# Performance work log

Measured on AMD Instinct MI355X. Metric: run time of the kernel, lower is better.

The kernel has to match this reference:

```python
import jax, jax.numpy as jnp
import numpy as np

HEADS = 7
DIM_HEAD = 64
SCALE = DIM_HEAD ** -0.5


def setup_inputs() -> dict:
    key = jax.random.key(0)
    ks = jax.random.split(key, 6)
    b, n, dim = 8, 1024, 448
    inner = HEADS * DIM_HEAD  # 448
    x = jax.random.normal(ks[0], (b, n, dim), dtype=jnp.float32)
    w_qv = jax.random.normal(ks[1], (dim, 2 * inner), dtype=jnp.float32) * 0.02
    ext_k = jax.random.normal(ks[2], (HEADS, n, DIM_HEAD), dtype=jnp.float32)
    ext_bias = jax.random.normal(ks[3], (HEADS, n, n), dtype=jnp.float32)
    w_out = jax.random.normal(ks[4], (inner, dim), dtype=jnp.float32) * 0.02
    b_out = jnp.zeros((dim,), dtype=jnp.float32)
    return {"x": x, "w_qv": w_qv, "ext_k": ext_k, "ext_bias": ext_bias,
            "w_out": w_out, "b_out": b_out}


def reference(x, w_qv, ext_k, ext_bias, w_out, b_out):
    b, n, dim = x.shape
    qv = x @ w_qv                                   # [b, n, 2*inner]
    q, v = jnp.split(qv, 2, axis=-1)
    # b n (h d) -> b h n d
    q = q.reshape(b, n, HEADS, DIM_HEAD).transpose(0, 2, 1, 3)
    v = v.reshape(b, n, HEADS, DIM_HEAD).transpose(0, 2, 1, 3)
    # scores vs external learned key, additive bias applied BEFORE scale
    dots = (jnp.einsum('bhnd,hmd->bhnm', q, ext_k) + ext_bias[None]) * SCALE
    attn = jax.nn.softmax(dots, axis=-1)
    out = jnp.einsum('bhnm,bhmd->bhnd', attn, v)
    out = out.transpose(0, 2, 1, 3).reshape(b, n, HEADS * DIM_HEAD)
    return out @ w_out + b_out  # dropout is identity in eval mode
```

## Files before the change

### kernel.cpp

```cpp
#include <hip/hip_runtime.h>
#include <hip/hip_bf16.h>
#include <hip/hip_fp16.h>

#define BATCH 8
#define NSEQ 1024
#define DIMM 448
#define NHEAD 7
#define HDIM 64
#define MROWS (BATCH*NSEQ)
#define KDIM 448
#define SCALE_F 0.125f

typedef short short8 __attribute__((ext_vector_type(8)));
typedef float floatx16 __attribute__((ext_vector_type(16)));

#define MFMA32(a,b,c) __builtin_amdgcn_mfma_f32_32x32x16_bf16(a,b,c,0,0,0)

__device__ __forceinline__ unsigned short f2bf(float f){
    __hip_bfloat16 h = __float2bfloat16(f);
    return *reinterpret_cast<unsigned short*>(&h);
}
__device__ __forceinline__ float bf2f(unsigned short u){
    __hip_bfloat16 h; *reinterpret_cast<unsigned short*>(&h) = u;
    return __bfloat162float(h);
}
__device__ __forceinline__ float h2f(unsigned short u){
    __half h; *reinterpret_cast<unsigned short*>(&h) = u;
    return __half2float(h);
}
__device__ __forceinline__ unsigned short f2h(float f){
    __half h = __float2half(f);
    return *reinterpret_cast<unsigned short*>(&h);
}

__global__ __launch_bounds__(256)
void prep_all(const float* __restrict__ x, const float* __restrict__ ek,
              const float* __restrict__ wqv, const float* __restrict__ wout,
              const float* __restrict__ eb,
              unsigned short* __restrict__ xh, unsigned short* __restrict__ ekh,
              unsigned short* __restrict__ wqvTh, unsigned short* __restrict__ woTh,
              unsigned short* __restrict__ woTl, unsigned short* __restrict__ bp)
{
    __shared__ float T[2][64][33];
    const int bx = blockIdx.x, tid = threadIdx.x;

    if (bx < 3584) {
        int i = bx*256 + tid;
        float4 v = ((const float4*)x)[i];
        ((ushort4*)xh)[i] = make_ushort4(f2bf(v.x), f2bf(v.y), f2bf(v.z), f2bf(v.w));
    } else if (bx < 4032) {
        int i = (bx-3584)*256 + tid;
        float4 v = ((const float4*)ek)[i];
        ((ushort4*)ekh)[i] = make_ushort4(f2bf(v.x), f2bf(v.y), f2bf(v.z), f2bf(v.w));
    } else if (bx < 4228) {
        int lid = (bx-4032)*4 + (tid>>6);
        int kc = lid % 56, ng = lid / 56;
        int n = ng*64 + (tid&63);
        unsigned short h[8];
#pragma unroll
        for (int j = 0; j < 8; ++j) h[j] = f2bf(wqv[(size_t)(kc*8+j)*896 + n]);
        size_t o = (size_t)n*KDIM + kc*8;
        *(ushort4*)(wqvTh + o)     = make_ushort4(h[0],h[1],h[2],h[3]);
        *(ushort4*)(wqvTh + o + 4) = make_ushort4(h[4],h[5],h[6],h[7]);
    } else if (bx < 4340) {
        int lid = (bx-4228)*4 + (tid>>6);
        int kc = lid % 56, ng = lid / 56;
        int n = ng*64 + (tid&63);
        ushort4 h0={0,0,0,0}, h1={0,0,0,0}, l0={0,0,0,0}, l1={0,0,0,0};
        if (n < DIMM) {
            unsigned short h[8], l[8];
#pragma unroll
            for (int j = 0; j < 8; ++j) {
                float f = wout[(size_t)(kc*8+j)*DIMM + n];
                h[j] = f2bf(f); l[j] = f2bf(f - bf2f(h[j]));
            }
            h0 = make_ushort4(h[0],h[1],h[2],h[3]); h1 = make_ushort4(h[4],h[5],h[6],h[7]);
            l0 = make_ushort4(l[0],l[1],l[2],l[3]); l1 = make_ushort4(l[4],l[5],l[6],l[7]);
        }
        size_t o = (size_t)n*KDIM + kc*8;
        *(ushort4*)(woTh + o) = h0; *(ushort4*)(woTh + o + 4) = h1;
        *(ushort4*)(woTl + o) = l0; *(ushort4*)(woTl + o + 4) = l1;
    } else {
        const int sub = tid >> 7, st = tid & 127;
        const int lid = (bx-4340)*2 + sub;
        const int mt = lid & 31, qt = (lid>>5) & 15, h = lid >> 9;
#pragma unroll
        for (int it = 0; it < 4; ++it) {
            int idx = it*128 + st;
            int row = idx >> 3, c4 = (idx & 7)*4;
            float4 v = *(const float4*)(eb + ((size_t)(h*NSEQ + qt*64 + row))*NSEQ + mt*32 + c4);
            T[sub][row][c4+0]=v.x; T[sub][row][c4+1]=v.y;
            T[sub][row][c4+2]=v.z; T[sub][row][c4+3]=v.w;
        }
        __syncthreads();
        const int g2 = st >> 6, lane = st & 63;
        const int lq = lane & 31, quad = lane >> 5;
        const int q = g2*32 + lq;
        unsigned short* dst = bp + ((((size_t)h*16 + qt)*32 + mt)*4 + g2*2)*512 + lane*8;
#pragma unroll
        for (int jj = 0; jj < 2; ++jj) {
            unsigned short o[8];
#pragma unroll
            for (int t = 0; t < 8; ++t) {
                int m = (t&3) + 8*(t>>2) + 16*jj + 4*quad;
                o[t] = f2h(T[sub][q][m] * SCALE_F);
            }
            *(ushort4*)(dst + jj*512)     = make_ushort4(o[0],o[1],o[2],o[3]);
            *(ushort4*)(dst + jj*512 + 4) = make_ushort4(o[4],o[5],o[6],o[7]);
        }
    }
}

__global__ __launch_bounds__(64, 2)
void gemm1_reg(const unsigned short* __restrict__ Ah, const unsigned short* __restrict__ Bh,
               unsigned short* __restrict__ qd, unsigned short* __restrict__ vTd)
{
    const int lane = threadIdx.x;
    const int lq = lane & 31, lh = lane >> 5;
    const int m0 = blockIdx.x * 64;
    const int y  = blockIdx.y;
    const int n0 = y * 64;
    const unsigned short* aB = Ah + (size_t)(m0 + lq)*KDIM + lh*8;
    const unsigned short* bB = Bh + (size_t)(n0 + lq)*KDIM + lh*8;

    floatx16 acc[2][2] = {};
    short8 aR[2][2][2], bR[2][2][2];
#define LD1(kt, par) {                                                        \
    _Pragma("unroll") for (int fm = 0; fm < 2; ++fm)                          \
    _Pragma("unroll") for (int c = 0; c < 2; ++c) {                           \
        aR[par][fm][c] = *(const short8*)(aB + (size_t)fm*32*KDIM + (kt)*32 + c*16); \
        bR[par][fm][c] = *(const short8*)(bB + (size_t)fm*32*KDIM + (kt)*32 + c*16); } }

    LD1(0, 0)
#pragma unroll
    for (int kt = 0; kt < 14; ++kt) {
        const int par = kt & 1;
        if (kt < 13) LD1(kt+1, par^1)
#pragma unroll
        for (int c = 0; c < 2; ++c)
#pragma unroll
            for (int fm = 0; fm < 2; ++fm)
#pragma unroll
                for (int fn = 0; fn < 2; ++fn)
                    acc[fm][fn] = MFMA32(aR[par][fm][c], bR[par][fn][c], acc[fm][fn]);
    }
#undef LD1

    if (y < NHEAD) {
#pragma unroll
        for (int fm = 0; fm < 2; ++fm)
#pragma unroll
            for (int fn = 0; fn < 2; ++fn) {
                const int d = fn*32 + lq;
#pragma unroll
                for (int r = 0; r < 16; ++r) {
                    const int gm = m0 + fm*32 + (r&3) + 8*(r>>2) + 4*lh;
                    const int b = gm >> 10, ns = gm & 1023;
                    qd[((size_t)((b*NHEAD + y)*NSEQ + ns))*HDIM + d] = f2bf(acc[fm][fn][r]);
                }
            }
    } else {
        const int head = y - NHEAD;
#pragma unroll
        for (int fm = 0; fm < 2; ++fm)
#pragma unroll
            for (int fn = 0; fn < 2; ++fn) {
                const int d = fn*32 + lq;
#pragma unroll
                for (int r = 0; r < 16; ++r) {
                    const int gm = m0 + fm*32 + (r&3) + 8*(r>>2) + 4*lh;
                    const int b = gm >> 10, ns = gm & 1023;
                    vTd[((size_t)((b*NHEAD + head)*HDIM + d))*NSEQ + ns] = f2bf(acc[fm][fn][r]);
                }
            }
    }
}

__global__ __launch_bounds__(64, 2)
void attn4(const unsigned short* __restrict__ qh_g, const unsigned short* __restrict__ vTh,
           const unsigned short* __restrict__ ekh, const unsigned short* __restrict__ bp,
           unsigned short* __restrict__ aoh, unsigned short* __restrict__ aol)
{
    __shared__ unsigned short pS[1024];
    __shared__ float linv[2][32];

    const int lane = threadIdx.x;
    const int lq = lane & 31, lh = lane >> 5;
    const int qt = blockIdx.x, head = blockIdx.y, b = blockIdx.z;
    const int bh = b*NHEAD + head;

    short8 qf[2][4];
#pragma unroll
    for (int g2 = 0; g2 < 2; ++g2)
#pragma unroll
        for (int c = 0; c < 4; ++c)
            qf[g2][c] = *(const short8*)(qh_g +
                ((size_t)(bh*NSEQ) + qt*64 + g2*32 + lq)*HDIM + c*16 + lh*8);

    const unsigned short* kB = ekh + ((size_t)head*NSEQ + lq)*HDIM + lh*8;
    const unsigned short* vB = vTh + ((size_t)(bh*HDIM) + lq)*NSEQ;
    const unsigned short* bB = bp + ((size_t)(head*16 + qt))*65536 + lane*8;

    short8 kR[2][4], vR[2][4], bR[2][4];
#define PREF(J, par) { const int mm = ((J) < 32) ? (J) : 0;                    \
    _Pragma("unroll") for (int c = 0; c < 4; ++c)                              \
        kR[par][c] = *(const short8*)(kB + (size_t)mm*2048 + c*16);            \
    _Pragma("unroll") for (int c2 = 0; c2 < 2; ++c2)                           \
    _Pragma("unroll") for (int h2 = 0; h2 < 2; ++h2)                           \
        vR[par][c2*2+h2] = *(const short8*)(vB + (size_t)(h2*32)*NSEQ + mm*32 + (c2*2+lh)*8); \
    _Pragma("unroll") for (int u = 0; u < 4; ++u)                              \
        bR[par][u] = *(const short8*)(bB + ((size_t)mm*4 + u)*512); }

    floatx16 O[2][2] = {};
    float ls[2] = {0.f, 0.f};

#define SEC(J, par, nxt) {                                                     \
    PREF((J)+1, nxt)                                                           \
    _Pragma("unroll") for (int g2 = 0; g2 < 2; ++g2) {                         \
        floatx16 S = {};                                                       \
        _Pragma("unroll") for (int c = 0; c < 4; ++c)                          \
            S = MFMA32(kR[par][c], qf[g2][c], S);                              \
        _Pragma("unroll") for (int g = 0; g < 4; ++g) {                        \
            unsigned short hb[4];                                              \
            _Pragma("unroll") for (int j2 = 0; j2 < 4; ++j2) {                 \
                const int i = g*4 + j2;                                        \
                float bs = h2f((unsigned short)bR[par][g2*2 + (i>>3)][i&7]);   \
                float pv = __expf(fmaf(S[i], SCALE_F, bs));                    \
                ls[g2] += pv;  hb[j2] = f2bf(pv);                              \
            }                                                                  \
            *(ushort4*)(pS + g*256 + lq*8 + lh*4) = make_ushort4(hb[0],hb[1],hb[2],hb[3]); \
        }                                                                      \
        _Pragma("unroll") for (int c2 = 0; c2 < 2; ++c2) {                     \
            short8 pf = *(const short8*)(pS + ((c2*2+lh)*32 + lq)*8);          \
            O[g2][0] = MFMA32(pf, vR[par][c2*2+0], O[g2][0]);                  \
            O[g2][1] = MFMA32(pf, vR[par][c2*2+1], O[g2][1]);                  \
        } } }

    PREF(0, 0)
    for (int jj = 0; jj < 16; ++jj) {
        SEC(2*jj,   0, 1)
        SEC(2*jj+1, 1, 0)
    }
#undef SEC
#undef PREF

    float lt0 = ls[0] + __shfl_xor(ls[0], 32);
    float lt1 = ls[1] + __shfl_xor(ls[1], 32);
    if (lh == 0) { linv[0][lq] = 1.f/lt0; linv[1][lq] = 1.f/lt1; }

#pragma unroll
    for (int g2 = 0; g2 < 2; ++g2)
#pragma unroll
        for (int r = 0; r < 16; ++r) {
            const int qr = (r&3) + 8*(r>>2) + 4*lh;
            const float inv = linv[g2][qr];
            const size_t o = ((size_t)(b*NSEQ) + qt*64 + g2*32 + qr)*DIMM + head*HDIM + lq;
            float v0 = O[g2][0][r]*inv, v1 = O[g2][1][r]*inv;
            unsigned short h0 = f2bf(v0), h1 = f2bf(v1);
            aoh[o]      = h0;  aol[o]      = f2bf(v0 - bf2f(h0));
            aoh[o + 32] = h1;  aol[o + 32] = f2bf(v1 - bf2f(h1));
        }
}

__global__ __launch_bounds__(64, 2)
void gemm2_reg(const unsigned short* __restrict__ Ah, const unsigned short* __restrict__ Al,
               const unsigned short* __restrict__ Bh, const unsigned short* __restrict__ Bl,
               const float* __restrict__ bias, float* __restrict__ out)
{
    const int lane = threadIdx.x;
    const int lq = lane & 31, lh = lane >> 5;
    const int m0 = blockIdx.x * 64;
    const int n0 = blockIdx.y * 64;
    const unsigned short* aBh = Ah + (size_t)(m0 + lq)*KDIM + lh*8;
    const unsigned short* aBl = Al + (size_t)(m0 + lq)*KDIM + lh*8;
    const unsigned short* bBh = Bh + (size_t)(n0 + lq)*KDIM + lh*8;
    const unsigned short* bBl = Bl + (size_t)(n0 + lq)*KDIM + lh*8;

    floatx16 acc[2][2] = {};
    short8 aH[2][2][2], aL[2][2][2], bH[2][2][2], bL[2][2][2];
#define LD2(kt, par) {                                                        \
    _Pragma("unroll") for (int fm = 0; fm < 2; ++fm)                          \
    _Pragma("unroll") for (int c = 0; c < 2; ++c) {                           \
        const size_t off = (size_t)fm*32*KDIM + (kt)*32 + c*16;               \
        aH[par][fm][c] = *(const short8*)(aBh + off);                         \
        aL[par][fm][c] = *(const short8*)(aBl + off);                         \
        bH[par][fm][c] = *(const short8*)(bBh + off);                         \
        bL[par][fm][c] = *(const short8*)(bBl + off); } }

    LD2(0, 0)
#pragma unroll
    for (int kt = 0; kt < 14; ++kt) {
        const int par = kt & 1;
        if (kt < 13) LD2(kt+1, par^1)
#pragma unroll
        for (int c = 0; c < 2; ++c)
#pragma unroll
            for (int fm = 0; fm < 2; ++fm)
#pragma unroll
                for (int fn = 0; fn < 2; ++fn) {
                    acc[fm][fn] = MFMA32(aH[par][fm][c], bH[par][fn][c], acc[fm][fn]);
                    acc[fm][fn] = MFMA32(aL[par][fm][c], bH[par][fn][c], acc[fm][fn]);
                    acc[fm][fn] = MFMA32(aH[par][fm][c], bL[par][fn][c], acc[fm][fn]);
                }
    }
#undef LD2

#pragma unroll
    for (int fm = 0; fm < 2; ++fm)
#pragma unroll
        for (int fn = 0; fn < 2; ++fn) {
            const int gn = n0 + fn*32 + lq;
            const float bv = bias[gn];
#pragma unroll
            for (int r = 0; r < 16; ++r) {
                const int gm = m0 + fm*32 + (r&3) + 8*(r>>2) + 4*lh;
                out[(size_t)gm*DIMM + gn] = acc[fm][fn][r] + bv;
            }
        }
}

extern "C" void kernel_launch(void* const* d_in, const int* in_sizes, int n_in,
                              void* d_out, int out_size, void* d_ws, size_t ws_size,
                              hipStream_t stream)
{
    const float* x    = (const float*)d_in[0];
    const float* wqv  = (const float*)d_in[1];
    const float* ek   = (const float*)d_in[2];
    const float* eb   = (const float*)d_in[3];
    const float* wout = (const float*)d_in[4];
    const float* bout = (const float*)d_in[5];
    float* out = (float*)d_out;

    const size_t MK = (size_t)MROWS*KDIM;
    const size_t EK = (size_t)NHEAD*NSEQ*HDIM;
    unsigned short* p = (unsigned short*)d_ws;
    unsigned short* xh    = p;  p += MK;
    unsigned short* wqvTh = p;  p += (size_t)896*KDIM;
    unsigned short* woTh  = p;  p += (size_t)512*KDIM;
    unsigned short* woTl  = p;  p += (size_t)512*KDIM;
    unsigned short* ekh   = p;  p += EK;
    unsigned short* qh    = p;  p += MK;
    unsigned short* vTh   = p;  p += MK;
    unsigned short* bp    = p;  p += (size_t)NHEAD*NSEQ*NSEQ;
    unsigned short* aoh   = p;  p += MK;
    unsigned short* aol   = p;  p += MK;

    prep_all<<<6132, 256, 0, stream>>>(x, ek, wqv, wout, eb,
                                       xh, ekh, wqvTh, woTh, woTl, bp);
    gemm1_reg<<<dim3(128, 14), 64, 0, stream>>>(xh, wqvTh, qh, vTh);
    attn4<<<dim3(16, NHEAD, BATCH), 64, 0, stream>>>(qh, vTh, ekh, bp, aoh, aol);
    gemm2_reg<<<dim3(128, 7), 64, 0, stream>>>(aoh, aol, woTh, woTl, bout, out);
}
```

Before: 201.4 us.

## Split attention blocks to 32 query rows each, doubling grid size

The attention kernel now gives each one-wave block a single 32-row query group instead of two, and launches twice as many blocks. This raises parallelism and cuts per-block register use (one score tile, half the output accumulators, half the bias fragments). In exchange, every block reloads the full external key and V tiles, so K/V global traffic doubles and each loaded K/V fragment feeds half as many MFMAs.

```diff
diff --git a/kernel.cpp b/kernel.cpp
--- a/kernel.cpp
+++ b/kernel.cpp
@@ -177,64 +177,63 @@
 }
 
 __global__ __launch_bounds__(64, 2)
-void attn4(const unsigned short* __restrict__ qh_g, const unsigned short* __restrict__ vTh,
+void attn5(const unsigned short* __restrict__ qh_g, const unsigned short* __restrict__ vTh,
            const unsigned short* __restrict__ ekh, const unsigned short* __restrict__ bp,
            unsigned short* __restrict__ aoh, unsigned short* __restrict__ aol)
 {
     __shared__ unsigned short pS[1024];
-    __shared__ float linv[2][32];
+    __shared__ float linv[32];
 
     const int lane = threadIdx.x;
     const int lq = lane & 31, lh = lane >> 5;
-    const int qt = blockIdx.x, head = blockIdx.y, b = blockIdx.z;
+    const int qt2 = blockIdx.x;
+    const int qt = qt2 >> 1, g2 = qt2 & 1;
+    const int head = blockIdx.y, b = blockIdx.z;
     const int bh = b*NHEAD + head;
 
-    short8 qf[2][4];
-#pragma unroll
-    for (int g2 = 0; g2 < 2; ++g2)
-#pragma unroll
-        for (int c = 0; c < 4; ++c)
-            qf[g2][c] = *(const short8*)(qh_g +
-                ((size_t)(bh*NSEQ) + qt*64 + g2*32 + lq)*HDIM + c*16 + lh*8);
+    short8 qf[4];
+#pragma unroll
+    for (int c = 0; c < 4; ++c)
+        qf[c] = *(const short8*)(qh_g +
+            ((size_t)(bh*NSEQ) + qt2*32 + lq)*HDIM + c*16 + lh*8);
 
     const unsigned short* kB = ekh + ((size_t)head*NSEQ + lq)*HDIM + lh*8;
     const unsigned short* vB = vTh + ((size_t)(bh*HDIM) + lq)*NSEQ;
-    const unsigned short* bB = bp + ((size_t)(head*16 + qt))*65536 + lane*8;
-
-    short8 kR[2][4], vR[2][4], bR[2][4];
+    const unsigned short* bB = bp + ((size_t)(head*16 + qt))*65536 + g2*1024 + lane*8;
+
+    short8 kR[2][4], vR[2][4], bR[2][2];
 #define PREF(J, par) { const int mm = ((J) < 32) ? (J) : 0;                    \
     _Pragma("unroll") for (int c = 0; c < 4; ++c)                              \
         kR[par][c] = *(const short8*)(kB + (size_t)mm*2048 + c*16);            \
     _Pragma("unroll") for (int c2 = 0; c2 < 2; ++c2)                           \
     _Pragma("unroll") for (int h2 = 0; h2 < 2; ++h2)                           \
         vR[par][c2*2+h2] = *(const short8*)(vB + (size_t)(h2*32)*NSEQ + mm*32 + (c2*2+lh)*8); \
-    _Pragma("unroll") for (int u = 0; u < 4; ++u)                              \
+    _Pragma("unroll") for (int u = 0; u < 2; ++u)                              \
         bR[par][u] = *(const short8*)(bB + ((size_t)mm*4 + u)*512); }
 
-    floatx16 O[2][2] = {};
-    float ls[2] = {0.f, 0.f};
+    floatx16 O[2] = {};
+    float ls = 0.f;
 
 #define SEC(J, par, nxt) {                                                     \
     PREF((J)+1, nxt)                                                           \
-    _Pragma("unroll") for (int g2 = 0; g2 < 2; ++g2) {                         \
-        floatx16 S = {};                                                       \
-        _Pragma("unroll") for (int c = 0; c < 4; ++c)                          \
-            S = MFMA32(kR[par][c], qf[g2][c], S);                              \
-        _Pragma("unroll") for (int g = 0; g < 4; ++g) {                        \
-            unsigned short hb[4];                                              \
-            _Pragma("unroll") for (int j2 = 0; j2 < 4; ++j2) {                 \
-                const int i = g*4 + j2;                                        \
-                float bs = h2f((unsigned short)bR[par][g2*2 + (i>>3)][i&7]);   \
-                float pv = __expf(fmaf(S[i], SCALE_F, bs));                    \
-                ls[g2] += pv;  hb[j2] = f2bf(pv);                              \
-            }                                                                  \
-            *(ushort4*)(pS + g*256 + lq*8 + lh*4) = make_ushort4(hb[0],hb[1],hb[2],hb[3]); \
+    floatx16 S = {};                                                           \
+    _Pragma("unroll") for (int c = 0; c < 4; ++c)                              \
+        S = MFMA32(kR[par][c], qf[c], S);                                      \
+    _Pragma("unroll") for (int g = 0; g < 4; ++g) {                            \
+        unsigned short hb[4];                                                  \
+        _Pragma("unroll") for (int j2 = 0; j2 < 4; ++j2) {                     \
+            const int i = g*4 + j2;                                            \
+            float bs = h2f((unsigned short)bR[par][i>>3][i&7]);                \
+            float pv = __expf(fmaf(S[i], SCALE_F, bs));                        \
+            ls += pv;  hb[j2] = f2bf(pv);                                      \
         }                                                                      \
-        _Pragma("unroll") for (int c2 = 0; c2 < 2; ++c2) {                     \
-            short8 pf = *(const short8*)(pS + ((c2*2+lh)*32 + lq)*8);          \
-            O[g2][0] = MFMA32(pf, vR[par][c2*2+0], O[g2][0]);                  \
-            O[g2][1] = MFMA32(pf, vR[par][c2*2+1], O[g2][1]);                  \
-        } } }
+        *(ushort4*)(pS + g*256 + lq*8 + lh*4) = make_ushort4(hb[0],hb[1],hb[2],hb[3]); \
+    }                                                                          \
+    _Pragma("unroll") for (int c2 = 0; c2 < 2; ++c2) {                         \
+        short8 pf = *(const short8*)(pS + ((c2*2+lh)*32 + lq)*8);              \
+        O[0] = MFMA32(pf, vR[par][c2*2+0], O[0]);                              \
+        O[1] = MFMA32(pf, vR[par][c2*2+1], O[1]);                              \
+    } }
 
     PREF(0, 0)
     for (int jj = 0; jj < 16; ++jj) {
@@ -244,22 +243,19 @@
 #undef SEC
 #undef PREF
 
-    float lt0 = ls[0] + __shfl_xor(ls[0], 32);
-    float lt1 = ls[1] + __shfl_xor(ls[1], 32);
-    if (lh == 0) { linv[0][lq] = 1.f/lt0; linv[1][lq] = 1.f/lt1; }
-
-#pragma unroll
-    for (int g2 = 0; g2 < 2; ++g2)
-#pragma unroll
-        for (int r = 0; r < 16; ++r) {
-            const int qr = (r&3) + 8*(r>>2) + 4*lh;
-            const float inv = linv[g2][qr];
-            const size_t o = ((size_t)(b*NSEQ) + qt*64 + g2*32 + qr)*DIMM + head*HDIM + lq;
-            float v0 = O[g2][0][r]*inv, v1 = O[g2][1][r]*inv;
-            unsigned short h0 = f2bf(v0), h1 = f2bf(v1);
-            aoh[o]      = h0;  aol[o]      = f2bf(v0 - bf2f(h0));
-            aoh[o + 32] = h1;  aol[o + 32] = f2bf(v1 - bf2f(h1));
-        }
+    float lt = ls + __shfl_xor(ls, 32);
+    if (lh == 0) linv[lq] = 1.f/lt;
+
+#pragma unroll
+    for (int r = 0; r < 16; ++r) {
+        const int qr = (r&3) + 8*(r>>2) + 4*lh;
+        const float inv = linv[qr];
+        const size_t o = ((size_t)(b*NSEQ) + qt2*32 + qr)*DIMM + head*HDIM + lq;
+        float v0 = O[0][r]*inv, v1 = O[1][r]*inv;
+        unsigned short h0 = f2bf(v0), h1 = f2bf(v1);
+        aoh[o]      = h0;  aol[o]      = f2bf(v0 - bf2f(h0));
+        aoh[o + 32] = h1;  aol[o + 32] = f2bf(v1 - bf2f(h1));
+    }
 }
 
 __global__ __launch_bounds__(64, 2)
@@ -348,6 +344,6 @@
     prep_all<<<6132, 256, 0, stream>>>(x, ek, wqv, wout, eb,
                                        xh, ekh, wqvTh, woTh, woTl, bp);
     gemm1_reg<<<dim3(128, 14), 64, 0, stream>>>(xh, wqvTh, qh, vTh);
-    attn4<<<dim3(16, NHEAD, BATCH), 64, 0, stream>>>(qh, vTh, ekh, bp, aoh, aol);
+    attn5<<<dim3(32, NHEAD, BATCH), 64, 0, stream>>>(qh, vTh, ekh, bp, aoh, aol);
     gemm2_reg<<<dim3(128, 7), 64, 0, stream>>>(aoh, aol, woTh, woTl, bout, out);
 }
```

Result: slower. 221.1 us (+9.8%).

## Split attention key dimension across four waves with LDS reduction

Applied to the files above, without the earlier changes.

The attention kernel moves from one wave per 64-query tile to four waves, each handling a quarter of the key sequence (8 of 32 chunks). Partial row sums and output accumulators are combined through shared memory, then one wave per output fragment normalizes and writes the result. This raises the number of waves in flight per tile, so memory latency in the long serial key loop is better hidden. In exchange it adds shared-memory reduction traffic and several block barriers.

```diff
diff --git a/kernel.cpp b/kernel.cpp
--- a/kernel.cpp
+++ b/kernel.cpp
@@ -176,18 +176,22 @@
     }
 }
 
-__global__ __launch_bounds__(64, 2)
-void attn4(const unsigned short* __restrict__ qh_g, const unsigned short* __restrict__ vTh,
+__global__ __launch_bounds__(256, 4)
+void attn6(const unsigned short* __restrict__ qh_g, const unsigned short* __restrict__ vTh,
            const unsigned short* __restrict__ ekh, const unsigned short* __restrict__ bp,
            unsigned short* __restrict__ aoh, unsigned short* __restrict__ aol)
 {
-    __shared__ unsigned short pS[1024];
-    __shared__ float linv[2][32];
-
-    const int lane = threadIdx.x;
+    __shared__ unsigned short pS[4][1024];
+    __shared__ float xch[3][64][17];
+    __shared__ float lsum[4][2][32];
+    __shared__ float linvS[2][32];
+
+    const int tid = threadIdx.x;
+    const int w = tid >> 6, lane = tid & 63;
     const int lq = lane & 31, lh = lane >> 5;
     const int qt = blockIdx.x, head = blockIdx.y, b = blockIdx.z;
     const int bh = b*NHEAD + head;
+    const int mBeg = w*8;
 
     short8 qf[2][4];
 #pragma unroll
@@ -202,7 +206,7 @@
     const unsigned short* bB = bp + ((size_t)(head*16 + qt))*65536 + lane*8;
 
     short8 kR[2][4], vR[2][4], bR[2][4];
-#define PREF(J, par) { const int mm = ((J) < 32) ? (J) : 0;                    \
+#define PREF(J, par) { const int mm = ((J) < mBeg+8) ? (J) : mBeg;             \
     _Pragma("unroll") for (int c = 0; c < 4; ++c)                              \
         kR[par][c] = *(const short8*)(kB + (size_t)mm*2048 + c*16);            \
     _Pragma("unroll") for (int c2 = 0; c2 < 2; ++c2)                           \
@@ -228,38 +232,60 @@
                 float pv = __expf(fmaf(S[i], SCALE_F, bs));                    \
                 ls[g2] += pv;  hb[j2] = f2bf(pv);                              \
             }                                                                  \
-            *(ushort4*)(pS + g*256 + lq*8 + lh*4) = make_ushort4(hb[0],hb[1],hb[2],hb[3]); \
+            *(ushort4*)(pS[w] + g*256 + lq*8 + lh*4) = make_ushort4(hb[0],hb[1],hb[2],hb[3]); \
         }                                                                      \
         _Pragma("unroll") for (int c2 = 0; c2 < 2; ++c2) {                     \
-            short8 pf = *(const short8*)(pS + ((c2*2+lh)*32 + lq)*8);          \
+            short8 pf = *(const short8*)(pS[w] + ((c2*2+lh)*32 + lq)*8);       \
             O[g2][0] = MFMA32(pf, vR[par][c2*2+0], O[g2][0]);                  \
             O[g2][1] = MFMA32(pf, vR[par][c2*2+1], O[g2][1]);                  \
         } } }
 
-    PREF(0, 0)
-    for (int jj = 0; jj < 16; ++jj) {
-        SEC(2*jj,   0, 1)
-        SEC(2*jj+1, 1, 0)
+    PREF(mBeg, 0)
+    for (int jj = 0; jj < 4; ++jj) {
+        SEC(mBeg+2*jj,   0, 1)
+        SEC(mBeg+2*jj+1, 1, 0)
     }
 #undef SEC
 #undef PREF
 
     float lt0 = ls[0] + __shfl_xor(ls[0], 32);
     float lt1 = ls[1] + __shfl_xor(ls[1], 32);
-    if (lh == 0) { linv[0][lq] = 1.f/lt0; linv[1][lq] = 1.f/lt1; }
-
-#pragma unroll
-    for (int g2 = 0; g2 < 2; ++g2)
-#pragma unroll
-        for (int r = 0; r < 16; ++r) {
-            const int qr = (r&3) + 8*(r>>2) + 4*lh;
-            const float inv = linv[g2][qr];
-            const size_t o = ((size_t)(b*NSEQ) + qt*64 + g2*32 + qr)*DIMM + head*HDIM + lq;
-            float v0 = O[g2][0][r]*inv, v1 = O[g2][1][r]*inv;
-            unsigned short h0 = f2bf(v0), h1 = f2bf(v1);
-            aoh[o]      = h0;  aol[o]      = f2bf(v0 - bf2f(h0));
-            aoh[o + 32] = h1;  aol[o + 32] = f2bf(v1 - bf2f(h1));
-        }
+    if (lh == 0) { lsum[w][0][lq] = lt0; lsum[w][1][lq] = lt1; }
+    __syncthreads();
+    if (w == 0) {
+        float t = lsum[0][lh][lq] + lsum[1][lh][lq] + lsum[2][lh][lq] + lsum[3][lh][lq];
+        linvS[lh][lq] = 1.f/t;
+    }
+    __syncthreads();
+
+#pragma unroll
+    for (int q = 0; q < 4; ++q) {
+        const int qg2 = q >> 1, qfn = q & 1;
+        if (w != q) {
+            const int slot = w - (w > q);
+#pragma unroll
+            for (int r = 0; r < 16; ++r) xch[slot][lane][r] = O[qg2][qfn][r];
+        }
+        __syncthreads();
+        if (w == q) {
+            floatx16 acc = O[qg2][qfn];
+#pragma unroll
+            for (int s = 0; s < 3; ++s)
+#pragma unroll
+                for (int r = 0; r < 16; ++r) acc[r] += xch[s][lane][r];
+#pragma unroll
+            for (int r = 0; r < 16; ++r) {
+                const int qr = (r&3) + 8*(r>>2) + 4*lh;
+                const float inv = linvS[qg2][qr];
+                const size_t o = ((size_t)(b*NSEQ) + qt*64 + qg2*32 + qr)*DIMM
+                               + head*HDIM + qfn*32 + lq;
+                float v = acc[r]*inv;
+                unsigned short h0 = f2bf(v);
+                aoh[o] = h0;  aol[o] = f2bf(v - bf2f(h0));
+            }
+        }
+        __syncthreads();
+    }
 }
 
 __global__ __launch_bounds__(64, 2)
@@ -348,6 +374,6 @@
     prep_all<<<6132, 256, 0, stream>>>(x, ek, wqv, wout, eb,
                                        xh, ekh, wqvTh, woTh, woTl, bp);
     gemm1_reg<<<dim3(128, 14), 64, 0, stream>>>(xh, wqvTh, qh, vTh);
-    attn4<<<dim3(16, NHEAD, BATCH), 64, 0, stream>>>(qh, vTh, ekh, bp, aoh, aol);
+    attn6<<<dim3(16, NHEAD, BATCH), 256, 0, stream>>>(qh, vTh, ekh, bp, aoh, aol);
     gemm2_reg<<<dim3(128, 7), 64, 0, stream>>>(aoh, aol, woTh, woTl, bout, out);
 }
```

Result: slower. 379.9 us (+88.6%).
